# Kernel tuning notes

Measured on AMD Instinct MI355X. Metric: run time of the kernel, lower is better.

The kernel has to match this reference:

```python
import jax, jax.numpy as jnp
import numpy as np

B, I, H, O, E, K = 1024, 512, 2048, 512, 8, 2


def setup_inputs() -> dict:
    key = jax.random.key(0)
    k = jax.random.split(key, 7)
    s = 0.02
    return {
        "x": jax.random.normal(k[0], (B, I), dtype=jnp.float32),
        "Wg": jax.random.normal(k[1], (I, E), dtype=jnp.float32) * s,
        "bg": jnp.zeros((E,), dtype=jnp.float32),
        "W1": jax.random.normal(k[2], (E, I, H), dtype=jnp.float32) * s,
        "b1": jnp.zeros((E, H), dtype=jnp.float32),
        "W2": jax.random.normal(k[3], (E, H, O), dtype=jnp.float32) * s,
        "b2": jnp.zeros((E, O), dtype=jnp.float32),
    }


def reference(x, Wg, bg, W1, b1, W2, b2):
    # Gating: linear -> softmax -> top-k -> renormalize (inference path,
    # no dynamic expert creation / sleep bookkeeping).
    logits = x @ Wg + bg                      # [B, E]
    probs = jax.nn.softmax(logits, axis=-1)
    top_w, top_i = jax.lax.top_k(probs, K)    # [B, K]
    top_w = top_w / jnp.sum(top_w, axis=-1, keepdims=True)
    # Dense combine weights: zero for unselected experts -> identical math to
    # the per-expert mask-gather / weighted scatter-add in the torch loop.
    combine = jnp.zeros((x.shape[0], W1.shape[0]), dtype=x.dtype)
    combine = combine.at[jnp.arange(x.shape[0])[:, None], top_i].add(top_w)  # [B, E]
    # Expert MLPs (Linear -> ReLU -> Linear), batched over experts.
    h = jax.nn.relu(jnp.einsum("bi,eih->beh", x, W1) + b1[None])  # [B, E, H]
    y = jnp.einsum("beh,eho->beo", h, W2) + b2[None]              # [B, E, O]
    out = jnp.einsum("be,beo->bo", combine, y)                    # [B, O]
    return out
```

## Files before the change

### kernel.cpp

```cpp
#include <hip/hip_runtime.h>
#include <math.h>


#define B_TOK 1024
#define I_DIM 512
#define H_DIM 2048
#define O_DIM 512
#define E_NUM 8

#define WS_COUNTS   0
#define WS_OFFSETS  32
#define WS_TOK_E    64
#define WS_TOK_W    8256
#define WS_SLOT_TOK 16448
#define WS_SLOT_WT  24640
#define WS_TOK_SLOT 32832
#define WS_XB       65536
#define WS_HB       (WS_XB + 1048576)
#define WS_Y4       (WS_HB + 8388608)

typedef __attribute__((ext_vector_type(8))) __bf16 bf16x8;
typedef __attribute__((ext_vector_type(4))) __bf16 bf16x4;
typedef __attribute__((ext_vector_type(4))) float f32x4;

#define MFMA16 __builtin_amdgcn_mfma_f32_16x16x32_bf16

__global__ __launch_bounds__(256) void gating_kernel(
    const float* __restrict__ x, const float* __restrict__ Wg,
    const float* __restrict__ bg, __bf16* __restrict__ xb,
    int* __restrict__ tok_e, float* __restrict__ tok_w)
{
    const int lane = threadIdx.x & 63;
    const int t = blockIdx.x * 4 + (threadIdx.x >> 6);
    const float4* x4 = (const float4*)(x + (size_t)t * I_DIM);
    float4 va = x4[lane], vb = x4[lane + 64];
    bf16x4 oa, ob;
    oa[0] = (__bf16)va.x; oa[1] = (__bf16)va.y;
    oa[2] = (__bf16)va.z; oa[3] = (__bf16)va.w;
    ob[0] = (__bf16)vb.x; ob[1] = (__bf16)vb.y;
    ob[2] = (__bf16)vb.z; ob[3] = (__bf16)vb.w;
    *(bf16x4*)(xb + (size_t)t * I_DIM + lane * 4) = oa;
    *(bf16x4*)(xb + (size_t)t * I_DIM + 256 + lane * 4) = ob;

    float acc[8];
#pragma unroll
    for (int e = 0; e < 8; ++e) acc[e] = 0.f;
    float xv[8] = {va.x, va.y, va.z, va.w, vb.x, vb.y, vb.z, vb.w};
#pragma unroll
    for (int u = 0; u < 8; ++u) {
        int i = (u < 4) ? (lane * 4 + u) : (256 + lane * 4 + u - 4);
        const float4* wr = (const float4*)(Wg + (size_t)i * 8);
        float4 wa = wr[0], wb2 = wr[1];
        acc[0] = fmaf(xv[u], wa.x, acc[0]);
        acc[1] = fmaf(xv[u], wa.y, acc[1]);
        acc[2] = fmaf(xv[u], wa.z, acc[2]);
        acc[3] = fmaf(xv[u], wa.w, acc[3]);
        acc[4] = fmaf(xv[u], wb2.x, acc[4]);
        acc[5] = fmaf(xv[u], wb2.y, acc[5]);
        acc[6] = fmaf(xv[u], wb2.z, acc[6]);
        acc[7] = fmaf(xv[u], wb2.w, acc[7]);
    }
#pragma unroll
    for (int off = 32; off > 0; off >>= 1)
#pragma unroll
        for (int e = 0; e < 8; ++e)
            acc[e] += __shfl_xor(acc[e], off, 64);
    if (lane == 0) {
        float l[8];
#pragma unroll
        for (int e = 0; e < 8; ++e) l[e] = acc[e] + bg[e];
        int e0 = 0;
        for (int e = 1; e < 8; ++e) if (l[e] > l[e0]) e0 = e;
        int e1 = (e0 == 0) ? 1 : 0;
        for (int e = 0; e < 8; ++e) {
            if (e == e0) continue;
            if (l[e] > l[e1]) e1 = e;
        }
        float w0 = 1.f / (1.f + expf(l[e1] - l[e0]));
        tok_e[t * 2]     = e0;
        tok_e[t * 2 + 1] = e1;
        tok_w[t * 2]     = w0;
        tok_w[t * 2 + 1] = 1.f - w0;
    }
}

__global__ __launch_bounds__(1024) void scatter_kernel(
    const int* __restrict__ tok_e, const float* __restrict__ tok_w,
    int* __restrict__ counts, int* __restrict__ offsets,
    int* __restrict__ slot_token, float* __restrict__ slot_wt,
    int* __restrict__ tok_slot)
{
    __shared__ int hist[8], soff[8], scur[8];
    const int tid = threadIdx.x;
    if (tid < 8) { hist[tid] = 0; scur[tid] = 0; }
    __syncthreads();
    const int e0 = tok_e[tid * 2], e1 = tok_e[tid * 2 + 1];
    atomicAdd(&hist[e0], 1);
    atomicAdd(&hist[e1], 1);
    __syncthreads();
    if (tid == 0) {
        int run = 0;
        for (int e = 0; e < 8; ++e) { soff[e] = run; run += hist[e]; }
    }
    __syncthreads();
    if (tid < 8) { counts[tid] = hist[tid]; offsets[tid] = soff[tid]; }
#pragma unroll
    for (int k = 0; k < 2; ++k) {
        int e = tok_e[tid * 2 + k];
        int pos = atomicAdd(&scur[e], 1);
        int slot = soff[e] + pos;
        slot_token[slot] = tid;
        slot_wt[slot] = tok_w[tid * 2 + k];
        tok_slot[tid * 2 + k] = slot;
    }
}

template <bool IS_FC1>
__global__ __launch_bounds__(256) void moe_gemm(
    const __bf16* __restrict__ A, const float* __restrict__ Wf,
    const float* __restrict__ bias,
    const int* __restrict__ counts, const int* __restrict__ offsets,
    const int* __restrict__ slot_token, float* __restrict__ y4,
    __bf16* __restrict__ hb)
{
    constexpr int N   = IS_FC1 ? H_DIM : O_DIM;
    constexpr int K   = IS_FC1 ? I_DIM : H_DIM;
    constexpr int BN  = IS_FC1 ? 32 : 64;
    constexpr int ITK = 4;

    const int e  = blockIdx.z;
    const int kc = IS_FC1 ? 0 : (int)blockIdx.y;
    const int n0 = blockIdx.x * BN;
    const int k0 = kc * 512;
    const int Me = counts[e];
    if (Me == 0) return;
    const int off = offsets[e];
    const float* W = Wf + (size_t)e * K * N;

    __shared__ __align__(16) __bf16 Bs[BN * 520];
    __shared__ __align__(16) __bf16 As[2][64 * 136];
    __shared__ __align__(16) unsigned char Sc[IS_FC1 ? 4096 : 16384];

    const int tid = threadIdx.x;
    const int lane = tid & 63, w = tid >> 6;

    {
        constexpr int KG = IS_FC1 ? 8 : 4;
        constexpr int KRUN = 512 / KG;
        const int bn = tid & (BN - 1);
        const int kg = tid / BN;
        const float* wp = W + (size_t)(k0 + kg * KRUN) * N + n0 + bn;
#pragma unroll 4
        for (int j = 0; j < KRUN / 4; ++j) {
            float v0 = wp[(size_t)(j * 4 + 0) * N];
            float v1 = wp[(size_t)(j * 4 + 1) * N];
            float v2 = wp[(size_t)(j * 4 + 2) * N];
            float v3 = wp[(size_t)(j * 4 + 3) * N];
            bf16x4 o;
            o[0] = (__bf16)v0; o[1] = (__bf16)v1;
            o[2] = (__bf16)v2; o[3] = (__bf16)v3;
            *(bf16x4*)&Bs[bn * 520 + kg * KRUN + j * 4] = o;
        }
    }
    __syncthreads();

    const int am = tid >> 2;
    const int ac = tid & 3;
    const int l15 = lane & 15, q = lane >> 4;
    const int wm = (w >> 1) * 32;
    const int wn = (w & 1) * (BN / 2);
    constexpr int NB = IS_FC1 ? 1 : 2;

    const __bf16* aptr;
    {
        int m = am; if (m >= Me) m = Me - 1;
        if (IS_FC1) aptr = A + (size_t)slot_token[off + m] * K;
        else        aptr = A + (size_t)(off + m) * K + k0;
    }
    bf16x8 ar[4];
#pragma unroll
    for (int j = 0; j < 4; ++j)
        ar[j] = *(const bf16x8*)(aptr + (ac + 4 * j) * 8);

    for (int m0 = 0; m0 < Me; m0 += 64) {
        f32x4 acc[2][NB] = {};
#pragma unroll
        for (int it = 0; it < ITK; ++it) {
            __bf16* as = As[it & 1];
#pragma unroll
            for (int j = 0; j < 4; ++j)
                *(bf16x8*)&as[am * 136 + (ac + 4 * j) * 8] = ar[j];
            __syncthreads();
            if (it + 1 < ITK) {
#pragma unroll
                for (int j = 0; j < 4; ++j)
                    ar[j] = *(const bf16x8*)(aptr + (it + 1) * 128 + (ac + 4 * j) * 8);
            } else if (m0 + 64 < Me) {
                int m = m0 + 64 + am; if (m >= Me) m = Me - 1;
                if (IS_FC1) aptr = A + (size_t)slot_token[off + m] * K;
                else        aptr = A + (size_t)(off + m) * K + k0;
#pragma unroll
                for (int j = 0; j < 4; ++j)
                    ar[j] = *(const bf16x8*)(aptr + (ac + 4 * j) * 8);
            }
#pragma unroll
            for (int ks = 0; ks < 4; ++ks) {
                bf16x8 af0 = *(const bf16x8*)&as[(wm + l15) * 136 + ks * 32 + q * 8];
                bf16x8 af1 = *(const bf16x8*)&as[(wm + 16 + l15) * 136 + ks * 32 + q * 8];
#pragma unroll
                for (int jj = 0; jj < NB; ++jj) {
                    bf16x8 bf = *(const bf16x8*)
                        &Bs[(wn + jj * 16 + l15) * 520 + it * 128 + ks * 32 + q * 8];
                    acc[0][jj] = MFMA16(af0, bf, acc[0][jj], 0, 0, 0);
                    acc[1][jj] = MFMA16(af1, bf, acc[1][jj], 0, 0, 0);
                }
            }
        }

        if (IS_FC1) {
            __bf16* sc = (__bf16*)Sc + w * 512;
            const int gn = n0 + wn + l15;
            const float bv = bias[e * H_DIM + gn];
#pragma unroll
            for (int i = 0; i < 2; ++i)
#pragma unroll
                for (int r = 0; r < 4; ++r) {
                    float v = acc[i][0][r] + bv;
                    sc[(i * 16 + q * 4 + r) * 16 + l15] = (__bf16)fmaxf(v, 0.f);
                }
            __syncthreads();
            int rr = lane >> 1, h = lane & 1;
            int m = m0 + wm + rr;
            if (m < Me) {
                bf16x8 vv = *(const bf16x8*)&sc[rr * 16 + h * 8];
                *(bf16x8*)&hb[(size_t)(off + m) * H_DIM + n0 + wn + h * 8] = vv;
            }
            __syncthreads();
        } else {
            float* sc = (float*)Sc + w * 1024;
#pragma unroll
            for (int jj = 0; jj < 2; ++jj)
#pragma unroll
                for (int i = 0; i < 2; ++i)
#pragma unroll
                    for (int r = 0; r < 4; ++r)
                        sc[(i * 16 + q * 4 + r) * 32 + jj * 16 + l15] = acc[i][jj][r];
            __syncthreads();
            int rr = lane >> 1, h = lane & 1;
            int m = m0 + wm + rr;
            if (m < Me) {
                float* dst = y4 + ((size_t)kc * 2048 + off + m) * O_DIM + n0 + wn + h * 16;
#pragma unroll
                for (int p = 0; p < 4; ++p)
                    *(float4*)(dst + p * 4) = *(const float4*)&sc[rr * 32 + h * 16 + p * 4];
            }
            __syncthreads();
        }
    }
}

__global__ __launch_bounds__(256) void combine_kernel(
    const float* __restrict__ y4, const float* __restrict__ b2,
    const int* __restrict__ tok_slot, const int* __restrict__ tok_e,
    const float* __restrict__ tok_w, float* __restrict__ out)
{
    const int idx = blockIdx.x * 256 + threadIdx.x;
    const int t = idx >> 7;
    const int c = (idx & 127) * 4;
    float4 sum = {0.f, 0.f, 0.f, 0.f};
#pragma unroll
    for (int k = 0; k < 2; ++k) {
        const int s = tok_slot[t * 2 + k];
        const int e = tok_e[t * 2 + k];
        const float wgt = tok_w[t * 2 + k];
        float4 a = *(const float4*)(b2 + (size_t)e * O_DIM + c);
#pragma unroll
        for (int kc = 0; kc < 4; ++kc) {
            float4 v = *(const float4*)(y4 + ((size_t)kc * 2048 + s) * O_DIM + c);
            a.x += v.x; a.y += v.y; a.z += v.z; a.w += v.w;
        }
        sum.x += wgt * a.x; sum.y += wgt * a.y;
        sum.z += wgt * a.z; sum.w += wgt * a.w;
    }
    *(float4*)(out + (size_t)t * O_DIM + c) = sum;
}

extern "C" void kernel_launch(void* const* d_in, const int* in_sizes, int n_in,
                              void* d_out, int out_size, void* d_ws, size_t ws_size,
                              hipStream_t stream)
{
    const float* x  = (const float*)d_in[0];
    const float* Wg = (const float*)d_in[1];
    const float* bg = (const float*)d_in[2];
    const float* W1 = (const float*)d_in[3];
    const float* b1 = (const float*)d_in[4];
    const float* W2 = (const float*)d_in[5];
    const float* b2 = (const float*)d_in[6];
    float* out = (float*)d_out;
    char* ws = (char*)d_ws;

    int*    counts   = (int*)(ws + WS_COUNTS);
    int*    offsets  = (int*)(ws + WS_OFFSETS);
    int*    tok_e    = (int*)(ws + WS_TOK_E);
    float*  tok_w    = (float*)(ws + WS_TOK_W);
    int*    slot_tok = (int*)(ws + WS_SLOT_TOK);
    float*  slot_wt  = (float*)(ws + WS_SLOT_WT);
    int*    tok_slot = (int*)(ws + WS_TOK_SLOT);
    __bf16* xb       = (__bf16*)(ws + WS_XB);
    __bf16* hb       = (__bf16*)(ws + WS_HB);
    float*  y4       = (float*)(ws + WS_Y4);
    (void)slot_wt;

    gating_kernel<<<B_TOK / 4, 256, 0, stream>>>(x, Wg, bg, xb, tok_e, tok_w);
    scatter_kernel<<<1, B_TOK, 0, stream>>>(tok_e, tok_w, counts, offsets,
                                            slot_tok, slot_wt, tok_slot);
    moe_gemm<true><<<dim3(64, 1, 8), 256, 0, stream>>>(
        xb, W1, b1, counts, offsets, slot_tok, y4, hb);
    moe_gemm<false><<<dim3(8, 4, 8), 256, 0, stream>>>(
        hb, W2, b2, counts, offsets, slot_tok, y4, hb);
    combine_kernel<<<(B_TOK * O_DIM / 4) / 256, 256, 0, stream>>>(
        y4, b2, tok_slot, tok_e, tok_w, out);
}
```

Measured before the change: 156.9 us.

## Restructure MoE GEMM to stream A fragments directly from global memory

The expert GEMM kernels no longer stage activation tiles in shared memory with double buffering and block-wide barriers. Each of 8 waves now handles its own 32-row strip and loads A fragments straight from global memory into MFMA operands, while only the weight tile stays in LDS. Blocks grow to 512 threads, the FC2 tile narrows to 32 columns so its grid doubles, and the LDS-staged coalesced epilogue becomes direct scalar stores. This removes barriers and LDS traffic but adds uncoalesced global A reads and scattered 2-byte and 4-byte output stores.

```diff
diff --git a/kernel.cpp b/kernel.cpp
--- a/kernel.cpp
+++ b/kernel.cpp
@@ -116,145 +116,102 @@
 }
 
 template <bool IS_FC1>
-__global__ __launch_bounds__(256) void moe_gemm(
+__global__ __launch_bounds__(512) void moe_gemm(
     const __bf16* __restrict__ A, const float* __restrict__ Wf,
     const float* __restrict__ bias,
     const int* __restrict__ counts, const int* __restrict__ offsets,
-    const int* __restrict__ slot_token, float* __restrict__ y4,
-    __bf16* __restrict__ hb)
-{
-    constexpr int N   = IS_FC1 ? H_DIM : O_DIM;
-    constexpr int K   = IS_FC1 ? I_DIM : H_DIM;
-    constexpr int BN  = IS_FC1 ? 32 : 64;
-    constexpr int ITK = 4;
+    const int* __restrict__ slot_token,
+    __bf16* __restrict__ hb, float* __restrict__ y4)
+{
+    constexpr int NW   = IS_FC1 ? H_DIM : O_DIM;
+    constexpr int KW   = IS_FC1 ? I_DIM : H_DIM;
+    constexpr int ASTR = IS_FC1 ? I_DIM : H_DIM;
 
     const int e  = blockIdx.z;
     const int kc = IS_FC1 ? 0 : (int)blockIdx.y;
-    const int n0 = blockIdx.x * BN;
     const int k0 = kc * 512;
+    const int n0 = blockIdx.x * 32;
     const int Me = counts[e];
     if (Me == 0) return;
     const int off = offsets[e];
-    const float* W = Wf + (size_t)e * K * N;
-
-    __shared__ __align__(16) __bf16 Bs[BN * 520];
-    __shared__ __align__(16) __bf16 As[2][64 * 136];
-    __shared__ __align__(16) unsigned char Sc[IS_FC1 ? 4096 : 16384];
+    const float* W = Wf + (size_t)e * KW * NW;
+
+    __shared__ __align__(16) __bf16 Bs[32 * 520];
 
     const int tid = threadIdx.x;
-    const int lane = tid & 63, w = tid >> 6;
-
     {
-        constexpr int KG = IS_FC1 ? 8 : 4;
-        constexpr int KRUN = 512 / KG;
-        const int bn = tid & (BN - 1);
-        const int kg = tid / BN;
-        const float* wp = W + (size_t)(k0 + kg * KRUN) * N + n0 + bn;
-#pragma unroll 4
-        for (int j = 0; j < KRUN / 4; ++j) {
-            float v0 = wp[(size_t)(j * 4 + 0) * N];
-            float v1 = wp[(size_t)(j * 4 + 1) * N];
-            float v2 = wp[(size_t)(j * 4 + 2) * N];
-            float v3 = wp[(size_t)(j * 4 + 3) * N];
+        const int bn = tid & 31;
+        const int kg = tid >> 5;
+        const float* wp = W + (size_t)(k0 + kg * 32) * NW + n0 + bn;
+#pragma unroll
+        for (int j4 = 0; j4 < 8; ++j4) {
+            float v0 = wp[(size_t)(j4 * 4 + 0) * NW];
+            float v1 = wp[(size_t)(j4 * 4 + 1) * NW];
+            float v2 = wp[(size_t)(j4 * 4 + 2) * NW];
+            float v3 = wp[(size_t)(j4 * 4 + 3) * NW];
             bf16x4 o;
             o[0] = (__bf16)v0; o[1] = (__bf16)v1;
             o[2] = (__bf16)v2; o[3] = (__bf16)v3;
-            *(bf16x4*)&Bs[bn * 520 + kg * KRUN + j * 4] = o;
-        }
-    }
-    __syncthreads();
-
-    const int am = tid >> 2;
-    const int ac = tid & 3;
+            *(bf16x4*)&Bs[bn * 520 + kg * 32 + j4 * 4] = o;
+        }
+    }
+    __syncthreads();
+
+    const int lane = tid & 63, w = tid >> 6;
     const int l15 = lane & 15, q = lane >> 4;
-    const int wm = (w >> 1) * 32;
-    const int wn = (w & 1) * (BN / 2);
-    constexpr int NB = IS_FC1 ? 1 : 2;
-
-    const __bf16* aptr;
-    {
-        int m = am; if (m >= Me) m = Me - 1;
-        if (IS_FC1) aptr = A + (size_t)slot_token[off + m] * K;
-        else        aptr = A + (size_t)(off + m) * K + k0;
-    }
-    bf16x8 ar[4];
-#pragma unroll
-    for (int j = 0; j < 4; ++j)
-        ar[j] = *(const bf16x8*)(aptr + (ac + 4 * j) * 8);
-
-    for (int m0 = 0; m0 < Me; m0 += 64) {
-        f32x4 acc[2][NB] = {};
-#pragma unroll
-        for (int it = 0; it < ITK; ++it) {
-            __bf16* as = As[it & 1];
-#pragma unroll
-            for (int j = 0; j < 4; ++j)
-                *(bf16x8*)&as[am * 136 + (ac + 4 * j) * 8] = ar[j];
-            __syncthreads();
-            if (it + 1 < ITK) {
-#pragma unroll
-                for (int j = 0; j < 4; ++j)
-                    ar[j] = *(const bf16x8*)(aptr + (it + 1) * 128 + (ac + 4 * j) * 8);
-            } else if (m0 + 64 < Me) {
-                int m = m0 + 64 + am; if (m >= Me) m = Me - 1;
-                if (IS_FC1) aptr = A + (size_t)slot_token[off + m] * K;
-                else        aptr = A + (size_t)(off + m) * K + k0;
-#pragma unroll
-                for (int j = 0; j < 4; ++j)
-                    ar[j] = *(const bf16x8*)(aptr + (ac + 4 * j) * 8);
+
+    for (int m0 = w * 32; m0 < Me; m0 += 256) {
+        int mA = m0 + l15;      if (mA >= Me) mA = Me - 1;
+        int mB = m0 + 16 + l15; if (mB >= Me) mB = Me - 1;
+        const __bf16 *a0, *a1;
+        if (IS_FC1) {
+            a0 = A + (size_t)slot_token[off + mA] * ASTR + q * 8;
+            a1 = A + (size_t)slot_token[off + mB] * ASTR + q * 8;
+        } else {
+            a0 = A + (size_t)(off + mA) * ASTR + k0 + q * 8;
+            a1 = A + (size_t)(off + mB) * ASTR + k0 + q * 8;
+        }
+
+        f32x4 acc[2][2] = {};
+#pragma unroll 4
+        for (int ks = 0; ks < 16; ++ks) {
+            bf16x8 af0 = *(const bf16x8*)(a0 + ks * 32);
+            bf16x8 af1 = *(const bf16x8*)(a1 + ks * 32);
+            bf16x8 bf0 = *(const bf16x8*)&Bs[l15 * 520 + ks * 32 + q * 8];
+            bf16x8 bf1 = *(const bf16x8*)&Bs[(16 + l15) * 520 + ks * 32 + q * 8];
+            acc[0][0] = MFMA16(af0, bf0, acc[0][0], 0, 0, 0);
+            acc[0][1] = MFMA16(af0, bf1, acc[0][1], 0, 0, 0);
+            acc[1][0] = MFMA16(af1, bf0, acc[1][0], 0, 0, 0);
+            acc[1][1] = MFMA16(af1, bf1, acc[1][1], 0, 0, 0);
+        }
+
+#pragma unroll
+        for (int jj = 0; jj < 2; ++jj) {
+            const int gn = n0 + jj * 16 + l15;
+            if (IS_FC1) {
+                const float bv = bias[e * H_DIM + gn];
+#pragma unroll
+                for (int i = 0; i < 2; ++i)
+#pragma unroll
+                    for (int r = 0; r < 4; ++r) {
+                        int m = m0 + i * 16 + q * 4 + r;
+                        if (m < Me) {
+                            float v = acc[i][jj][r] + bv;
+                            hb[(size_t)(off + m) * H_DIM + gn] =
+                                (__bf16)fmaxf(v, 0.f);
+                        }
+                    }
+            } else {
+#pragma unroll
+                for (int i = 0; i < 2; ++i)
+#pragma unroll
+                    for (int r = 0; r < 4; ++r) {
+                        int m = m0 + i * 16 + q * 4 + r;
+                        if (m < Me)
+                            y4[((size_t)kc * 2048 + off + m) * O_DIM + gn] =
+                                acc[i][jj][r];
+                    }
             }
-#pragma unroll
-            for (int ks = 0; ks < 4; ++ks) {
-                bf16x8 af0 = *(const bf16x8*)&as[(wm + l15) * 136 + ks * 32 + q * 8];
-                bf16x8 af1 = *(const bf16x8*)&as[(wm + 16 + l15) * 136 + ks * 32 + q * 8];
-#pragma unroll
-                for (int jj = 0; jj < NB; ++jj) {
-                    bf16x8 bf = *(const bf16x8*)
-                        &Bs[(wn + jj * 16 + l15) * 520 + it * 128 + ks * 32 + q * 8];
-                    acc[0][jj] = MFMA16(af0, bf, acc[0][jj], 0, 0, 0);
-                    acc[1][jj] = MFMA16(af1, bf, acc[1][jj], 0, 0, 0);
-                }
-            }
-        }
-
-        if (IS_FC1) {
-            __bf16* sc = (__bf16*)Sc + w * 512;
-            const int gn = n0 + wn + l15;
-            const float bv = bias[e * H_DIM + gn];
-#pragma unroll
-            for (int i = 0; i < 2; ++i)
-#pragma unroll
-                for (int r = 0; r < 4; ++r) {
-                    float v = acc[i][0][r] + bv;
-                    sc[(i * 16 + q * 4 + r) * 16 + l15] = (__bf16)fmaxf(v, 0.f);
-                }
-            __syncthreads();
-            int rr = lane >> 1, h = lane & 1;
-            int m = m0 + wm + rr;
-            if (m < Me) {
-                bf16x8 vv = *(const bf16x8*)&sc[rr * 16 + h * 8];
-                *(bf16x8*)&hb[(size_t)(off + m) * H_DIM + n0 + wn + h * 8] = vv;
-            }
-            __syncthreads();
-        } else {
-            float* sc = (float*)Sc + w * 1024;
-#pragma unroll
-            for (int jj = 0; jj < 2; ++jj)
-#pragma unroll
-                for (int i = 0; i < 2; ++i)
-#pragma unroll
-                    for (int r = 0; r < 4; ++r)
-                        sc[(i * 16 + q * 4 + r) * 32 + jj * 16 + l15] = acc[i][jj][r];
-            __syncthreads();
-            int rr = lane >> 1, h = lane & 1;
-            int m = m0 + wm + rr;
-            if (m < Me) {
-                float* dst = y4 + ((size_t)kc * 2048 + off + m) * O_DIM + n0 + wn + h * 16;
-#pragma unroll
-                for (int p = 0; p < 4; ++p)
-                    *(float4*)(dst + p * 4) = *(const float4*)&sc[rr * 32 + h * 16 + p * 4];
-            }
-            __syncthreads();
         }
     }
 }
@@ -309,15 +266,14 @@
     __bf16* xb       = (__bf16*)(ws + WS_XB);
     __bf16* hb       = (__bf16*)(ws + WS_HB);
     float*  y4       = (float*)(ws + WS_Y4);
-    (void)slot_wt;
 
     gating_kernel<<<B_TOK / 4, 256, 0, stream>>>(x, Wg, bg, xb, tok_e, tok_w);
     scatter_kernel<<<1, B_TOK, 0, stream>>>(tok_e, tok_w, counts, offsets,
                                             slot_tok, slot_wt, tok_slot);
-    moe_gemm<true><<<dim3(64, 1, 8), 256, 0, stream>>>(
-        xb, W1, b1, counts, offsets, slot_tok, y4, hb);
-    moe_gemm<false><<<dim3(8, 4, 8), 256, 0, stream>>>(
-        hb, W2, b2, counts, offsets, slot_tok, y4, hb);
+    moe_gemm<true><<<dim3(64, 1, 8), 512, 0, stream>>>(
+        xb, W1, b1, counts, offsets, slot_tok, hb, y4);
+    moe_gemm<false><<<dim3(16, 4, 8), 512, 0, stream>>>(
+        hb, W2, b2, counts, offsets, slot_tok, hb, y4);
     combine_kernel<<<(B_TOK * O_DIM / 4) / 256, 256, 0, stream>>>(
         y4, b2, tok_slot, tok_e, tok_w, out);
 }
```

New measurement: 158.6 us. About the same (+1.1%).
